# Optimization experiments

Measured on AMD Instinct MI355X. Metric: run time of the kernel, lower is better.

The kernel has to match this reference:

```python
import jax, jax.numpy as jnp
import numpy as np

THRESH = 0.5
SCALE_POS = 2.0
SCALE_NEG = 40.0


def setup_inputs() -> dict:
    key = jax.random.key(0)
    k1, k2, k3, k4 = jax.random.split(key, 4)
    N, M, D, C = 8192, 8192, 256, 100
    emb_img = jax.random.normal(k1, (N, D), dtype=jnp.float32)
    emb_text = jax.random.normal(k2, (M, D), dtype=jnp.float32)
    # L2-normalize: cosine similarities in [-1,1], as the thresh/scale values assume
    emb_img = emb_img / jnp.linalg.norm(emb_img, axis=-1, keepdims=True)
    emb_text = emb_text / jnp.linalg.norm(emb_text, axis=-1, keepdims=True)
    gt_pre = jax.random.randint(k3, (N,), 0, C, dtype=jnp.int64 if jax.config.jax_enable_x64 else jnp.int32).astype(jnp.int32)
    gt_pres_map = jax.random.randint(k4, (M,), 0, C, dtype=jnp.int32)
    return {"emb_img": emb_img, "emb_text": emb_text, "gt_pre": gt_pre, "gt_pres_map": gt_pres_map}


def reference(emb_img, emb_text, gt_pre, gt_pres_map):
    # [N, M] pairwise similarity
    matrix = jnp.matmul(emb_img, emb_text.T)
    # vectorized equivalent of the nested python loop: z[i,j] = (gt_pre[i] == gt_pres_map[j])
    z = gt_pre[:, None] == gt_pres_map[None, :]
    # matrix_p = z*matrix; kept entries are where z==1 AND matrix>0 (same for negatives with 1-z)
    pos_mask = z & (matrix > 0)
    neg_mask = (~z) & (matrix > 0)
    pos_cnt = jnp.sum(pos_mask)
    neg_cnt = jnp.sum(neg_mask)
    pos_sum = jnp.sum(jnp.where(pos_mask, jnp.exp(-SCALE_POS * (matrix - THRESH)), 0.0))
    neg_sum = jnp.sum(jnp.where(neg_mask, jnp.exp(SCALE_NEG * (matrix - THRESH)), 0.0))
    pos_loss = jnp.where(
        pos_cnt > 0,
        jnp.log1p(pos_sum) / (SCALE_POS * jnp.maximum(pos_cnt, 1).astype(matrix.dtype)),
        jnp.zeros((), matrix.dtype),
    )
    neg_loss = jnp.where(
        neg_cnt > 0,
        jnp.log1p(neg_sum) / (SCALE_NEG * jnp.maximum(neg_cnt, 1).astype(matrix.dtype)),
        jnp.zeros((), matrix.dtype),
    )
    return pos_loss + neg_loss
```

## Files before the change

### kernel.cpp

```cpp
#include <hip/hip_runtime.h>
#include <hip/hip_bf16.h>
#include <math.h>

#define N_IMG 8192
#define M_TXT 8192
#define DIMK  256
#define BT    128
#define BK    32

typedef short bf16x8 __attribute__((ext_vector_type(8)));
typedef float f32x4  __attribute__((ext_vector_type(4)));

__device__ inline void gload_lds16(const void* g, void* l) {
    __builtin_amdgcn_global_load_lds(
        (const __attribute__((address_space(1))) unsigned int*)g,
        (__attribute__((address_space(3))) unsigned int*)l,
        16, 0, 0);
}

__device__ inline unsigned short f2bf(float x) {
    unsigned u = __float_as_uint(x);
    u += 0x7FFFu + ((u >> 16) & 1u);
    return (unsigned short)(u >> 16);
}

__global__ void convert_swz(const float* __restrict__ srcA,
                            const float* __restrict__ srcB,
                            unsigned short* __restrict__ dstA,
                            unsigned short* __restrict__ dstB,
                            double* __restrict__ accums) {
    if (blockIdx.x == 0) {
#pragma unroll
        for (int s = 0; s < 8; ++s) accums[threadIdx.x * 8 + s] = 0.0;
    }
    int q = blockIdx.x * blockDim.x + threadIdx.x;
    const int per = N_IMG * (DIMK / 8);
    const float* src; unsigned short* dst; int qq = q;
    if (q < per) { src = srcA; dst = dstA; }
    else         { src = srcB; dst = dstB; qq = q - per; }
    int r  = qq >> 5, jj = qq & 31;
    int kb = jj >> 2, j = jj & 3;
    int c  = (j - (r >> 1)) & 3;
    const float4* s = (const float4*)(src + (size_t)r * DIMK + kb * 32 + c * 8);
    float4 a = s[0], b = s[1];
    uint4 w;
    w.x = (unsigned)f2bf(a.x) | ((unsigned)f2bf(a.y) << 16);
    w.y = (unsigned)f2bf(a.z) | ((unsigned)f2bf(a.w) << 16);
    w.z = (unsigned)f2bf(b.x) | ((unsigned)f2bf(b.y) << 16);
    w.w = (unsigned)f2bf(b.z) | ((unsigned)f2bf(b.w) << 16);
    ((uint4*)dst)[qq] = w;
}

__launch_bounds__(256, 4)
__global__ void msloss_gemm(const unsigned short* __restrict__ Abf,
                            const unsigned short* __restrict__ Bbf,
                            const int* __restrict__ rowLab,
                            const int* __restrict__ colLab,
                            double* __restrict__ accums) {
    __shared__ __align__(16) unsigned short As[2][BT * BK];
    __shared__ __align__(16) unsigned short Bs[2][BT * BK];

    int tid  = threadIdx.x;
    int wave = tid >> 6, lane = tid & 63;
    int r16  = lane & 15, kg = lane >> 4;
    int wrow = (wave >> 1) * 64, wcol = (wave & 1) * 64;

    int swz = (blockIdx.x & 7) * 512 + (blockIdx.x >> 3);
    int tileRow = (swz >> 6) * BT;
    int tileCol = (swz & 63) * BT;

    int tr = tileRow + wrow, tc = tileCol + wcol;
    int4 rl4[4]; int mycl[4];
#pragma unroll
    for (int m = 0; m < 4; ++m)
        rl4[m] = *(const int4*)(rowLab + tr + m * 16 + kg * 4);
#pragma unroll
    for (int n = 0; n < 4; ++n)
        mycl[n] = colLab[tc + n * 16 + r16];

    auto STAGE = [&](int sel, int k0) {
#pragma unroll
        for (int i = 0; i < 2; ++i) {
            int p = wave * 128 + i * 64 + lane;
            int r = p >> 2, j = p & 3;
            gload_lds16(Abf + (size_t)(tileRow + r) * DIMK + k0 + j * 8,
                        &As[sel][(wave * 128 + i * 64) * 8]);
        }
#pragma unroll
        for (int i = 0; i < 2; ++i) {
            int p = wave * 128 + i * 64 + lane;
            int r = p >> 2, j = p & 3;
            gload_lds16(Bbf + (size_t)(tileCol + r) * DIMK + k0 + j * 8,
                        &Bs[sel][(wave * 128 + i * 64) * 8]);
        }
    };

    f32x4 acc[4][4] = {};

    STAGE(0, 0);

#pragma unroll 1
    for (int t = 0; t < DIMK / BK; ++t) {
        if (t < DIMK / BK - 1) {
            STAGE((t + 1) & 1, (t + 1) * BK);
            asm volatile("s_waitcnt vmcnt(4)" ::: "memory");
        } else {
            asm volatile("s_waitcnt vmcnt(0)" ::: "memory");
        }
        __builtin_amdgcn_s_barrier();
        __builtin_amdgcn_sched_barrier(0);

        const unsigned short* as = As[t & 1];
        const unsigned short* bs = Bs[t & 1];
        int slot = ((r16 >> 1) + kg) & 3;
        bf16x8 a[4], b[4];
#pragma unroll
        for (int m = 0; m < 4; ++m)
            a[m] = *(const bf16x8*)(as + (wrow + m * 16 + r16) * BK + slot * 8);
#pragma unroll
        for (int n = 0; n < 4; ++n)
            b[n] = *(const bf16x8*)(bs + (wcol + n * 16 + r16) * BK + slot * 8);
#pragma unroll
        for (int m = 0; m < 4; ++m)
#pragma unroll
            for (int n = 0; n < 4; ++n)
                acc[m][n] = __builtin_amdgcn_mfma_f32_16x16x32_bf16(
                    a[m], b[n], acc[m][n], 0, 0, 0);

        asm volatile("s_waitcnt lgkmcnt(0)" ::: "memory");
        __builtin_amdgcn_sched_barrier(0);
        __builtin_amdgcn_s_barrier();
    }

    const float CPOS = -2.8853900817779268f;
    const float CNEG = 57.707801635558536f;
    const float DPOS = 1.4426950408889634f;
    const float DNEG = -28.853900817779268f;
    const float THI  = 0.25f;

    float ps = 0.f, ns = 0.f;
    unsigned posc = 0, pec = 0;
#pragma unroll
    for (int m = 0; m < 4; ++m) {
        int lab[4] = {rl4[m].x, rl4[m].y, rl4[m].z, rl4[m].w};
#pragma unroll
        for (int j = 0; j < 4; ++j) {
            int myrl = lab[j];
#pragma unroll
            for (int n = 0; n < 4; ++n) {
                float v  = acc[m][n][j];
                bool eq  = (myrl == mycl[n]);
                bool pos = v > 0.f;
                unsigned long long bp  = __ballot(pos);
                unsigned long long bpe = bp & __ballot(eq);
                unsigned long long bhi = __ballot(v > THI);
                posc += (unsigned)__popcll(bp);
                pec  += (unsigned)__popcll(bpe);
                if (__builtin_expect((bool)(bpe | bhi), 0)) {
                    float targ = fmaf(v, eq ? CPOS : CNEG, eq ? DPOS : DNEG);
                    float e    = exp2f(pos ? targ : -100.f);
                    bool  pe   = pos && eq;
                    ps += pe ? e : 0.f;
                    ns += pe ? 0.f : e;
                }
            }
        }
    }
#pragma unroll
    for (int off = 32; off > 0; off >>= 1) {
        ps += __shfl_down(ps, off, 64);
        ns += __shfl_down(ns, off, 64);
    }
    if (lane == 0) {
        double* s = accums + ((((unsigned)blockIdx.x << 2) | (unsigned)wave) & 255u) * 8;
        atomicAdd(s + 0, (double)ps);
        atomicAdd(s + 1, (double)ns);
        atomicAdd((unsigned long long*)(s + 2), (unsigned long long)pec);
        atomicAdd((unsigned long long*)(s + 3), (unsigned long long)(posc - pec));
    }
}

__global__ void finalize_loss(const double* __restrict__ accums,
                              float* __restrict__ out) {
    int lane = threadIdx.x;
    double ps = 0, ns = 0, pc = 0, nc = 0;
#pragma unroll
    for (int s = lane; s < 256; s += 64) {
        ps += accums[s * 8 + 0];
        ns += accums[s * 8 + 1];
        pc += (double)((const unsigned long long*)accums)[s * 8 + 2];
        nc += (double)((const unsigned long long*)accums)[s * 8 + 3];
    }
#pragma unroll
    for (int off = 32; off > 0; off >>= 1) {
        ps += __shfl_down(ps, off, 64);
        ns += __shfl_down(ns, off, 64);
        pc += __shfl_down(pc, off, 64);
        nc += __shfl_down(nc, off, 64);
    }
    if (lane == 0) {
        double pl = (pc > 0.0) ? log1p(ps) / (2.0 * pc)  : 0.0;
        double nl = (nc > 0.0) ? log1p(ns) / (40.0 * nc) : 0.0;
        out[0] = (float)(pl + nl);
    }
}

extern "C" void kernel_launch(void* const* d_in, const int* in_sizes, int n_in,
                              void* d_out, int out_size, void* d_ws, size_t ws_size,
                              hipStream_t stream) {
    (void)in_sizes; (void)n_in; (void)out_size;
    const float* img    = (const float*)d_in[0];
    const float* txt    = (const float*)d_in[1];
    const int*   gt_pre = (const int*)d_in[2];
    const int*   gt_map = (const int*)d_in[3];
    float* out = (float*)d_out;

    const size_t ACC_BYTES = 256 * 8 * sizeof(double);
    const size_t MAT_BYTES = (size_t)N_IMG * DIMK * 2;
    if (ws_size < ACC_BYTES + 2 * MAT_BYTES) return;

    double*         accums = (double*)d_ws;
    unsigned short* Abf = (unsigned short*)((char*)d_ws + ACC_BYTES);
    unsigned short* Bbf = (unsigned short*)((char*)d_ws + ACC_BYTES + MAT_BYTES);

    int nchunks = 2 * N_IMG * (DIMK / 8);
    convert_swz<<<nchunks / 256, 256, 0, stream>>>(img, txt, Abf, Bbf, accums);
    msloss_gemm<<<(N_IMG / BT) * (M_TXT / BT), 256, 0, stream>>>(Abf, Bbf, gt_pre, gt_map, accums);
    finalize_loss<<<1, 64, 0, stream>>>(accums, out);
}
```

Before: 75.58 us.

## Make GEMM persistent with per-group atomic tile tickets and fused finalize

```diff
diff --git a/kernel.cpp b/kernel.cpp
--- a/kernel.cpp
+++ b/kernel.cpp
@@ -7,6 +7,8 @@
 #define DIMK  256
 #define BT    128
 #define BK    32
+#define GRID  768
+#define TPG   512
 
 typedef short bf16x8 __attribute__((ext_vector_type(8)));
 typedef float f32x4  __attribute__((ext_vector_type(4)));
@@ -28,10 +30,13 @@
                             const float* __restrict__ srcB,
                             unsigned short* __restrict__ dstA,
                             unsigned short* __restrict__ dstB,
-                            double* __restrict__ accums) {
+                            double* __restrict__ accums,
+                            int* __restrict__ ctl) {
     if (blockIdx.x == 0) {
 #pragma unroll
         for (int s = 0; s < 8; ++s) accums[threadIdx.x * 8 + s] = 0.0;
+        if (threadIdx.x < 8)  ctl[threadIdx.x * 32] = GRID / 8;
+        if (threadIdx.x == 8) ctl[256] = 0;
     }
     int q = blockIdx.x * blockDim.x + threadIdx.x;
     const int per = N_IMG * (DIMK / 8);
@@ -51,86 +56,63 @@
     ((uint4*)dst)[qq] = w;
 }
 
-__launch_bounds__(256, 4)
+__launch_bounds__(256, 3)
 __global__ void msloss_gemm(const unsigned short* __restrict__ Abf,
                             const unsigned short* __restrict__ Bbf,
                             const int* __restrict__ rowLab,
                             const int* __restrict__ colLab,
-                            double* __restrict__ accums) {
+                            double* __restrict__ accums,
+                            int* __restrict__ ctl,
+                            float* __restrict__ out) {
     __shared__ __align__(16) unsigned short As[2][BT * BK];
     __shared__ __align__(16) unsigned short Bs[2][BT * BK];
+    __shared__ int sNext;
 
     int tid  = threadIdx.x;
     int wave = tid >> 6, lane = tid & 63;
     int r16  = lane & 15, kg = lane >> 4;
     int wrow = (wave >> 1) * 64, wcol = (wave & 1) * 64;
 
-    int swz = (blockIdx.x & 7) * 512 + (blockIdx.x >> 3);
-    int tileRow = (swz >> 6) * BT;
-    int tileCol = (swz & 63) * BT;
-
-    int tr = tileRow + wrow, tc = tileCol + wcol;
-    int4 rl4[4]; int mycl[4];
-#pragma unroll
-    for (int m = 0; m < 4; ++m)
-        rl4[m] = *(const int4*)(rowLab + tr + m * 16 + kg * 4);
-#pragma unroll
-    for (int n = 0; n < 4; ++n)
-        mycl[n] = colLab[tc + n * 16 + r16];
-
-    auto STAGE = [&](int sel, int k0) {
+    int bid = blockIdx.x;
+    int grp = bid & 7;
+    int* ticket  = ctl + grp * 32;
+    int* doneCnt = ctl + 256;
+
+    auto COORD = [&](int idxv, int& rr, int& cc) {
+        int swz = grp * TPG + idxv;
+        rr = (swz >> 6) * BT;
+        cc = (swz & 63) * BT;
+    };
+    auto STAGE = [&](int sel, int k0, int trow, int tcol) {
 #pragma unroll
         for (int i = 0; i < 2; ++i) {
             int p = wave * 128 + i * 64 + lane;
             int r = p >> 2, j = p & 3;
-            gload_lds16(Abf + (size_t)(tileRow + r) * DIMK + k0 + j * 8,
+            gload_lds16(Abf + (size_t)(trow + r) * DIMK + k0 + j * 8,
                         &As[sel][(wave * 128 + i * 64) * 8]);
         }
 #pragma unroll
         for (int i = 0; i < 2; ++i) {
             int p = wave * 128 + i * 64 + lane;
             int r = p >> 2, j = p & 3;
-            gload_lds16(Bbf + (size_t)(tileCol + r) * DIMK + k0 + j * 8,
+            gload_lds16(Bbf + (size_t)(tcol + r) * DIMK + k0 + j * 8,
                         &Bs[sel][(wave * 128 + i * 64) * 8]);
         }
     };
 
-    f32x4 acc[4][4] = {};
-
-    STAGE(0, 0);
-
-#pragma unroll 1
-    for (int t = 0; t < DIMK / BK; ++t) {
-        if (t < DIMK / BK - 1) {
-            STAGE((t + 1) & 1, (t + 1) * BK);
-            asm volatile("s_waitcnt vmcnt(4)" ::: "memory");
-        } else {
-            asm volatile("s_waitcnt vmcnt(0)" ::: "memory");
-        }
-        __builtin_amdgcn_s_barrier();
-        __builtin_amdgcn_sched_barrier(0);
-
-        const unsigned short* as = As[t & 1];
-        const unsigned short* bs = Bs[t & 1];
-        int slot = ((r16 >> 1) + kg) & 3;
-        bf16x8 a[4], b[4];
+    int idx = bid >> 3;
+    int tileRow, tileCol;
+    COORD(idx, tileRow, tileCol);
+
+    int4 rl4[4], rl4n[4]; int mycl[4], mycln[4];
+    auto LOADLAB = [&](int trow, int tcol, int4* R, int* C) {
 #pragma unroll
         for (int m = 0; m < 4; ++m)
-            a[m] = *(const bf16x8*)(as + (wrow + m * 16 + r16) * BK + slot * 8);
+            R[m] = *(const int4*)(rowLab + trow + wrow + m * 16 + kg * 4);
 #pragma unroll
         for (int n = 0; n < 4; ++n)
-            b[n] = *(const bf16x8*)(bs + (wcol + n * 16 + r16) * BK + slot * 8);
-#pragma unroll
-        for (int m = 0; m < 4; ++m)
-#pragma unroll
-            for (int n = 0; n < 4; ++n)
-                acc[m][n] = __builtin_amdgcn_mfma_f32_16x16x32_bf16(
-                    a[m], b[n], acc[m][n], 0, 0, 0);
-
-        asm volatile("s_waitcnt lgkmcnt(0)" ::: "memory");
-        __builtin_amdgcn_sched_barrier(0);
-        __builtin_amdgcn_s_barrier();
-    }
+            C[n] = colLab[tcol + wcol + n * 16 + r16];
+    };
 
     const float CPOS = -2.8853900817779268f;
     const float CNEG = 57.707801635558536f;
@@ -138,70 +120,153 @@
     const float DNEG = -28.853900817779268f;
     const float THI  = 0.25f;
 
-    float ps = 0.f, ns = 0.f;
-    unsigned posc = 0, pec = 0;
-#pragma unroll
-    for (int m = 0; m < 4; ++m) {
-        int lab[4] = {rl4[m].x, rl4[m].y, rl4[m].z, rl4[m].w};
-#pragma unroll
-        for (int j = 0; j < 4; ++j) {
-            int myrl = lab[j];
-#pragma unroll
-            for (int n = 0; n < 4; ++n) {
-                float v  = acc[m][n][j];
-                bool eq  = (myrl == mycl[n]);
-                bool pos = v > 0.f;
-                unsigned long long bp  = __ballot(pos);
-                unsigned long long bpe = bp & __ballot(eq);
-                unsigned long long bhi = __ballot(v > THI);
-                posc += (unsigned)__popcll(bp);
-                pec  += (unsigned)__popcll(bpe);
-                if (__builtin_expect((bool)(bpe | bhi), 0)) {
-                    float targ = fmaf(v, eq ? CPOS : CNEG, eq ? DPOS : DNEG);
-                    float e    = exp2f(pos ? targ : -100.f);
-                    bool  pe   = pos && eq;
-                    ps += pe ? e : 0.f;
-                    ns += pe ? 0.f : e;
+    STAGE(0, 0, tileRow, tileCol);
+    LOADLAB(tileRow, tileCol, rl4, mycl);
+
+    bool first = true;
+    int nIdx = TPG, tkt = TPG;
+    int slot = ((r16 >> 1) + kg) & 3;
+
+    for (;;) {
+        f32x4 acc[4][4] = {};
+        int nRow = 0, nCol = 0;
+
+#pragma unroll 1
+        for (int t = 0; t < 8; ++t) {
+            if (t < 7) {
+                STAGE((t + 1) & 1, (t + 1) * BK, tileRow, tileCol);
+            } else if (nIdx < TPG) {
+                COORD(nIdx, nRow, nCol);
+                STAGE(0, 0, nRow, nCol);
+                LOADLAB(nRow, nCol, rl4n, mycln);
+            }
+            if (t == 0) {
+                if (first) asm volatile("s_waitcnt vmcnt(12)" ::: "memory");
+                else       asm volatile("s_waitcnt vmcnt(16)" ::: "memory");
+            } else if (t < 7) {
+                asm volatile("s_waitcnt vmcnt(4)" ::: "memory");
+            } else if (nIdx < TPG) {
+                asm volatile("s_waitcnt vmcnt(12)" ::: "memory");
+            } else {
+                asm volatile("s_waitcnt vmcnt(0)" ::: "memory");
+            }
+            __builtin_amdgcn_s_barrier();
+            __builtin_amdgcn_sched_barrier(0);
+
+            if (t == 1 && tid == 0)
+                tkt = atomicAdd(ticket, 1);
+
+            const unsigned short* as = As[t & 1];
+            const unsigned short* bs = Bs[t & 1];
+            bf16x8 a[4], b[4];
+#pragma unroll
+            for (int m = 0; m < 4; ++m)
+                a[m] = *(const bf16x8*)(as + (wrow + m * 16 + r16) * BK + slot * 8);
+#pragma unroll
+            for (int n = 0; n < 4; ++n)
+                b[n] = *(const bf16x8*)(bs + (wcol + n * 16 + r16) * BK + slot * 8);
+#pragma unroll
+            for (int m = 0; m < 4; ++m)
+#pragma unroll
+                for (int n = 0; n < 4; ++n)
+                    acc[m][n] = __builtin_amdgcn_mfma_f32_16x16x32_bf16(
+                        a[m], b[n], acc[m][n], 0, 0, 0);
+
+            if (t == 2 && tid == 0) sNext = tkt;
+
+            asm volatile("s_waitcnt lgkmcnt(0)" ::: "memory");
+            __builtin_amdgcn_sched_barrier(0);
+            __builtin_amdgcn_s_barrier();
+
+            if (t == 2) nIdx = sNext;
+        }
+
+        float ps = 0.f, ns = 0.f;
+        unsigned posc = 0, pec = 0;
+#pragma unroll
+        for (int m = 0; m < 4; ++m) {
+            int lab[4] = {rl4[m].x, rl4[m].y, rl4[m].z, rl4[m].w};
+#pragma unroll
+            for (int j = 0; j < 4; ++j) {
+                int myrl = lab[j];
+#pragma unroll
+                for (int n = 0; n < 4; ++n) {
+                    float v  = acc[m][n][j];
+                    bool eq  = (myrl == mycl[n]);
+                    bool pos = v > 0.f;
+                    unsigned long long bp  = __ballot(pos);
+                    unsigned long long bpe = bp & __ballot(eq);
+                    unsigned long long bhi = __ballot(v > THI);
+                    posc += (unsigned)__popcll(bp);
+                    pec  += (unsigned)__popcll(bpe);
+                    if (__builtin_expect((bool)(bpe | bhi), 0)) {
+                        float targ = fmaf(v, eq ? CPOS : CNEG, eq ? DPOS : DNEG);
+                        float e    = exp2f(pos ? targ : -100.f);
+                        bool  pe   = pos && eq;
+                        ps += pe ? e : 0.f;
+                        ns += pe ? 0.f : e;
+                    }
                 }
             }
         }
+#pragma unroll
+        for (int off = 32; off > 0; off >>= 1) {
+            ps += __shfl_down(ps, off, 64);
+            ns += __shfl_down(ns, off, 64);
+        }
+        if (lane == 0) {
+            double* s = accums + ((((unsigned)bid << 2) | (unsigned)wave) & 255u) * 8;
+            atomicAdd(s + 0, (double)ps);
+            atomicAdd(s + 1, (double)ns);
+            atomicAdd((unsigned long long*)(s + 2), (unsigned long long)pec);
+            atomicAdd((unsigned long long*)(s + 3), (unsigned long long)(posc - pec));
+        }
+
+        if (nIdx >= TPG) break;
+        tileRow = nRow; tileCol = nCol;
+#pragma unroll
+        for (int m = 0; m < 4; ++m) rl4[m] = rl4n[m];
+#pragma unroll
+        for (int n = 0; n < 4; ++n) mycl[n] = mycln[n];
+        first = false;
     }
-#pragma unroll
-    for (int off = 32; off > 0; off >>= 1) {
-        ps += __shfl_down(ps, off, 64);
-        ns += __shfl_down(ns, off, 64);
-    }
-    if (lane == 0) {
-        double* s = accums + ((((unsigned)blockIdx.x << 2) | (unsigned)wave) & 255u) * 8;
-        atomicAdd(s + 0, (double)ps);
-        atomicAdd(s + 1, (double)ns);
-        atomicAdd((unsigned long long*)(s + 2), (unsigned long long)pec);
-        atomicAdd((unsigned long long*)(s + 3), (unsigned long long)(posc - pec));
-    }
-}
-
-__global__ void finalize_loss(const double* __restrict__ accums,
-                              float* __restrict__ out) {
-    int lane = threadIdx.x;
-    double ps = 0, ns = 0, pc = 0, nc = 0;
-#pragma unroll
-    for (int s = lane; s < 256; s += 64) {
-        ps += accums[s * 8 + 0];
-        ns += accums[s * 8 + 1];
-        pc += (double)((const unsigned long long*)accums)[s * 8 + 2];
-        nc += (double)((const unsigned long long*)accums)[s * 8 + 3];
-    }
-#pragma unroll
-    for (int off = 32; off > 0; off >>= 1) {
-        ps += __shfl_down(ps, off, 64);
-        ns += __shfl_down(ns, off, 64);
-        pc += __shfl_down(pc, off, 64);
-        nc += __shfl_down(nc, off, 64);
-    }
-    if (lane == 0) {
-        double pl = (pc > 0.0) ? log1p(ps) / (2.0 * pc)  : 0.0;
-        double nl = (nc > 0.0) ? log1p(ns) / (40.0 * nc) : 0.0;
-        out[0] = (float)(pl + nl);
+
+    asm volatile("s_waitcnt vmcnt(0)" ::: "memory");
+    __builtin_amdgcn_s_barrier();
+    if (wave == 0) {
+        int old = 0;
+        if (lane == 0)
+            old = __hip_atomic_fetch_add(doneCnt, 1, __ATOMIC_ACQ_REL,
+                                         __HIP_MEMORY_SCOPE_AGENT);
+        old = __shfl(old, 0, 64);
+        if (old == GRID - 1) {
+            double fps = 0, fns = 0, fpc = 0, fnc = 0;
+#pragma unroll
+            for (int s = lane; s < 256; s += 64) {
+                fps += __hip_atomic_load(&accums[s * 8 + 0], __ATOMIC_RELAXED,
+                                         __HIP_MEMORY_SCOPE_AGENT);
+                fns += __hip_atomic_load(&accums[s * 8 + 1], __ATOMIC_RELAXED,
+                                         __HIP_MEMORY_SCOPE_AGENT);
+                fpc += (double)__hip_atomic_load(
+                    (unsigned long long*)&accums[s * 8 + 2], __ATOMIC_RELAXED,
+                    __HIP_MEMORY_SCOPE_AGENT);
+                fnc += (double)__hip_atomic_load(
+                    (unsigned long long*)&accums[s * 8 + 3], __ATOMIC_RELAXED,
+                    __HIP_MEMORY_SCOPE_AGENT);
+            }
+#pragma unroll
+            for (int off = 32; off > 0; off >>= 1) {
+                fps += __shfl_down(fps, off, 64);
+                fns += __shfl_down(fns, off, 64);
+                fpc += __shfl_down(fpc, off, 64);
+                fnc += __shfl_down(fnc, off, 64);
+            }
+            if (lane == 0) {
+                double pl = (fpc > 0.0) ? log1p(fps) / (2.0 * fpc)  : 0.0;
+                double nl = (fnc > 0.0) ? log1p(fns) / (40.0 * fnc) : 0.0;
+                out[0] = (float)(pl + nl);
+            }
+        }
     }
 }
 
@@ -216,15 +281,16 @@
     float* out = (float*)d_out;
 
     const size_t ACC_BYTES = 256 * 8 * sizeof(double);
+    const size_t CTL_BYTES = 2048;
     const size_t MAT_BYTES = (size_t)N_IMG * DIMK * 2;
-    if (ws_size < ACC_BYTES + 2 * MAT_BYTES) return;
-
-    double*         accums = (double*)d_ws;
-    unsigned short* Abf = (unsigned short*)((char*)d_ws + ACC_BYTES);
-    unsigned short* Bbf = (unsigned short*)((char*)d_ws + ACC_BYTES + MAT_BYTES);
+    if (ws_size < ACC_BYTES + CTL_BYTES + 2 * MAT_BYTES) return;
+
+    double* accums = (double*)d_ws;
+    int*    ctl    = (int*)((char*)d_ws + ACC_BYTES);
+    unsigned short* Abf = (unsigned short*)((char*)d_ws + ACC_BYTES + CTL_BYTES);
+    unsigned short* Bbf = (unsigned short*)((char*)d_ws + ACC_BYTES + CTL_BYTES + MAT_BYTES);
 
     int nchunks = 2 * N_IMG * (DIMK / 8);
-    convert_swz<<<nchunks / 256, 256, 0, stream>>>(img, txt, Abf, Bbf, accums);
-    msloss_gemm<<<(N_IMG / BT) * (M_TXT / BT), 256, 0, stream>>>(Abf, Bbf, gt_pre, gt_map, accums);
-    finalize_loss<<<1, 64, 0, stream>>>(accums, out);
-}
+    convert_swz<<<nchunks / 256, 256, 0, stream>>>(img, txt, Abf, Bbf, accums, ctl);
+    msloss_gemm<<<GRID, 256, 0, stream>>>(Abf, Bbf, gt_pre, gt_map, accums, ctl, out);
+}
```

Result: slower. 92.40 us (+22.3%).
